# Kernel optimization log

Hardware: AMD Instinct MI355X
Metric: run time of the kernel (lower is better)

## Reference

```python
import jax, jax.numpy as jnp
import numpy as np

EMBED_DIM = 2048
NUM_HEADS = 16
HEAD_DIM = EMBED_DIM // NUM_HEADS
SEQ_LEN = 2048
ROPE_BASE = 10000.0


def rope_cache(seq_len, dim, base=ROPE_BASE):
    inv_freq = 1.0 / (base ** (jnp.arange(0, dim, 2, dtype=jnp.float32) / dim))
    t = jnp.arange(seq_len, dtype=jnp.float32)
    freqs = jnp.einsum('s,d->sd', t, inv_freq)  # [S, D/2]
    return jnp.cos(freqs), jnp.sin(freqs)


def apply_rope_interleaved(x, cos, sin):
    # x: [B, S, H, D]; interleaved pairs (even, odd)
    B, S, H, D = x.shape
    xp = x.reshape(B, S, H, D // 2, 2)
    x1, x2 = xp[..., 0], xp[..., 1]
    c = cos[None, :, None, :]
    s = sin[None, :, None, :]
    o1 = x1 * c - x2 * s
    o2 = x1 * s + x2 * c
    return jnp.stack([o1, o2], axis=-1).reshape(B, S, H, D)


def setup_inputs() -> dict:
    key = jax.random.key(0)
    ks = jax.random.split(key, 5)
    B = 2
    scale = 0.02
    x = jax.random.normal(ks[0], (B, SEQ_LEN, EMBED_DIM), dtype=jnp.float32)
    Wq = jax.random.normal(ks[1], (EMBED_DIM, EMBED_DIM), dtype=jnp.float32) * scale
    Wk = jax.random.normal(ks[2], (EMBED_DIM, EMBED_DIM), dtype=jnp.float32) * scale
    Wv = jax.random.normal(ks[3], (EMBED_DIM, EMBED_DIM), dtype=jnp.float32) * scale
    Wo = jax.random.normal(ks[4], (EMBED_DIM, EMBED_DIM), dtype=jnp.float32) * scale
    return {"x": x, "Wq": Wq, "Wk": Wk, "Wv": Wv, "Wo": Wo}


def reference(x, Wq, Wk, Wv, Wo):
    B, S, E = x.shape
    H, D = NUM_HEADS, HEAD_DIM
    # projections (nn.Linear: y = x @ W.T; here W stored as [out, in])
    q = (x @ Wq.T).reshape(B, S, H, D)
    k = (x @ Wk.T).reshape(B, S, H, D)
    v = (x @ Wv.T).reshape(B, S, H, D)
    cos, sin = rope_cache(S, D)
    q = apply_rope_interleaved(q, cos, sin)
    k = apply_rope_interleaved(k, cos, sin)
    # causal attention, flash-attn semantics: scale = head_dim**-0.5, fp32 softmax
    scale = 1.0 / jnp.sqrt(jnp.float32(D))
    scores = jnp.einsum('bqhd,bkhd->bhqk', q, k) * scale
    causal = jnp.tril(jnp.ones((S, S), dtype=bool))
    scores = jnp.where(causal[None, None], scores, jnp.float32(-jnp.inf))
    probs = jax.nn.softmax(scores.astype(jnp.float32), axis=-1)
    attn = jnp.einsum('bhqk,bkhd->bqhd', probs.astype(v.dtype), v)
    attn = attn.reshape(B, S, H * D)
    return attn @ Wo.T
```

## Files before the change

kernel.cpp:

```cpp
#include <hip/hip_runtime.h>
#include <cstdint>
#include <cmath>

typedef short s16x8 __attribute__((ext_vector_type(8)));
typedef float f32x4 __attribute__((ext_vector_type(4)));
typedef float f32x16 __attribute__((ext_vector_type(16)));
typedef int   i32x4 __attribute__((ext_vector_type(4)));
typedef unsigned short u16;

#define E_DIM 2048
#define SEQ   2048
#define NB    2
#define NH    16
#define HD    128
#define BS_TOT 4096

__device__ __forceinline__ u16 f2bf(float f) {
  unsigned u = __float_as_uint(f);
  u += 0x7fffu + ((u >> 16) & 1u);
  return (u16)(u >> 16);
}
__device__ __forceinline__ float bf2f(u16 h) {
  return __uint_as_float(((unsigned)h) << 16);
}
__device__ __forceinline__ float rmax16(float v) {
  v = fmaxf(v, __shfl_xor(v, 1));
  v = fmaxf(v, __shfl_xor(v, 2));
  v = fmaxf(v, __shfl_xor(v, 4));
  v = fmaxf(v, __shfl_xor(v, 8));
  return v;
}
__device__ __forceinline__ float rsum16(float v) {
  v += __shfl_xor(v, 1);
  v += __shfl_xor(v, 2);
  v += __shfl_xor(v, 4);
  v += __shfl_xor(v, 8);
  return v;
}

__device__ __forceinline__ void gll16(const u16* g, u16* l) {
  __builtin_amdgcn_global_load_lds(
      (const __attribute__((address_space(1))) void*)g,
      (__attribute__((address_space(3))) void*)l, 16, 0, 0);
}

__global__ __launch_bounds__(256) void cast_kernel(const float* __restrict__ in,
                                                   u16* __restrict__ out) {
  const size_t t = (size_t)blockIdx.x * 256 + threadIdx.x;
  const float* p = in + t * 8;
  f32x4 a = *(const f32x4*)p;
  f32x4 b = *(const f32x4*)(p + 4);
  union { u16 u[8]; i32x4 v; } r;
  r.u[0] = f2bf(a[0]); r.u[1] = f2bf(a[1]); r.u[2] = f2bf(a[2]); r.u[3] = f2bf(a[3]);
  r.u[4] = f2bf(b[0]); r.u[5] = f2bf(b[1]); r.u[6] = f2bf(b[2]); r.u[7] = f2bf(b[3]);
  *(i32x4*)(out + t * 8) = r.v;
}

__global__ __launch_bounds__(256) void cast2_kernel(const float* __restrict__ in0,
                                                    u16* __restrict__ out0,
                                                    const float* __restrict__ in1,
                                                    u16* __restrict__ out1,
                                                    int half) {
  const int bsel = blockIdx.x >= half;
  const float* in = bsel ? in1 : in0;
  u16* out = bsel ? out1 : out0;
  const size_t t = (size_t)(blockIdx.x - (bsel ? half : 0)) * 256 + threadIdx.x;
  const float* p = in + t * 8;
  f32x4 a = *(const f32x4*)p;
  f32x4 b = *(const f32x4*)(p + 4);
  union { u16 u[8]; i32x4 v; } r;
  r.u[0] = f2bf(a[0]); r.u[1] = f2bf(a[1]); r.u[2] = f2bf(a[2]); r.u[3] = f2bf(a[3]);
  r.u[4] = f2bf(b[0]); r.u[5] = f2bf(b[1]); r.u[6] = f2bf(b[2]); r.u[7] = f2bf(b[3]);
  *(i32x4*)(out + t * 8) = r.v;
}

template <typename OT, bool CVTA>
__global__ __launch_bounds__(256) void gemm_nt(const void* __restrict__ Av,
                                               const u16* __restrict__ B,
                                               OT* __restrict__ C,
                                               int M, int N, int K) {
  __shared__ __align__(16) u16 As[128 * 64];
  __shared__ __align__(16) u16 Bs[128 * 64];
  const int t  = threadIdx.x;
  const int w  = t >> 6, l = t & 63;
  const int l31 = l & 31, lh = l >> 5;
  const int wr = w >> 1, wc = w & 1;
  const int m0 = blockIdx.y * 128, n0 = blockIdx.x * 128;

  f32x16 acc[2][2];
#pragma unroll
  for (int mi = 0; mi < 2; ++mi)
#pragma unroll
    for (int ni = 0; ni < 2; ++ni)
#pragma unroll
      for (int e = 0; e < 16; ++e) acc[mi][ni][e] = 0.f;

  for (int k0 = 0; k0 < K; k0 += 64) {
    __syncthreads();
    if constexpr (CVTA) {
      const float* A = (const float*)Av;
#pragma unroll
      for (int i = 0; i < 4; ++i) {
        const int ci = i * 256 + t;
        const int r = ci >> 3, c = ci & 7, gq = c ^ (r & 7);
        const float* s = A + (size_t)(m0 + r) * K + k0 + gq * 8;
        f32x4 a = *(const f32x4*)s;
        f32x4 b = *(const f32x4*)(s + 4);
        union { u16 u[8]; i32x4 v; } rr;
        rr.u[0] = f2bf(a[0]); rr.u[1] = f2bf(a[1]); rr.u[2] = f2bf(a[2]); rr.u[3] = f2bf(a[3]);
        rr.u[4] = f2bf(b[0]); rr.u[5] = f2bf(b[1]); rr.u[6] = f2bf(b[2]); rr.u[7] = f2bf(b[3]);
        *(i32x4*)(As + ci * 8) = rr.v;
      }
    } else {
      const u16* A = (const u16*)Av;
#pragma unroll
      for (int i = 0; i < 4; ++i) {
        const int ci = i * 256 + t;
        const int r = ci >> 3, c = ci & 7, gq = c ^ (r & 7);
        gll16(A + (size_t)(m0 + r) * K + k0 + gq * 8, As + ci * 8);
      }
    }
#pragma unroll
    for (int i = 0; i < 4; ++i) {
      const int ci = i * 256 + t;
      const int r = ci >> 3, c = ci & 7, gq = c ^ (r & 7);
      gll16(B + (size_t)(n0 + r) * K + k0 + gq * 8, Bs + ci * 8);
    }
    __syncthreads();
#pragma unroll
    for (int ks = 0; ks < 4; ++ks) {
      const int chunk = ks * 2 + lh;
      s16x8 af[2], bf[2];
#pragma unroll
      for (int mi = 0; mi < 2; ++mi) {
        const int ra = wr * 64 + mi * 32 + l31;
        af[mi] = *(const s16x8*)(As + ra * 64 + ((chunk ^ (ra & 7)) << 3));
      }
#pragma unroll
      for (int ni = 0; ni < 2; ++ni) {
        const int rb = wc * 64 + ni * 32 + l31;
        bf[ni] = *(const s16x8*)(Bs + rb * 64 + ((chunk ^ (rb & 7)) << 3));
      }
#pragma unroll
      for (int mi = 0; mi < 2; ++mi)
#pragma unroll
        for (int ni = 0; ni < 2; ++ni)
          acc[mi][ni] = __builtin_amdgcn_mfma_f32_32x32x16_bf16(af[mi], bf[ni], acc[mi][ni], 0, 0, 0);
    }
  }

#pragma unroll
  for (int mi = 0; mi < 2; ++mi)
#pragma unroll
    for (int ni = 0; ni < 2; ++ni) {
      const int col = n0 + wc * 64 + ni * 32 + l31;
#pragma unroll
      for (int reg = 0; reg < 16; ++reg) {
        const int row = m0 + wr * 64 + mi * 32 + 4 * lh + (reg & 3) + 8 * (reg >> 2);
        const float v = acc[mi][ni][reg];
        if constexpr (sizeof(OT) == 2) {
          C[(size_t)row * N + col] = (OT)f2bf(v);
        } else {
          C[(size_t)row * N + col] = v;
        }
      }
    }
}

__global__ __launch_bounds__(256) void gemm_qk(const u16* __restrict__ A,
                                               const u16* __restrict__ B0,
                                               const u16* __restrict__ B1,
                                               u16* __restrict__ C0,
                                               u16* __restrict__ C1) {
  constexpr int K = 2048, N = 2048;
  __shared__ __align__(16) u16 As[128 * 64];
  __shared__ __align__(16) u16 Bs[128 * 64];
  const int bx = blockIdx.x;
  const u16* B = (bx >> 4) ? B1 : B0;
  u16* C = (bx >> 4) ? C1 : C0;
  const int n0 = (bx & 15) * 128, m0 = blockIdx.y * 128;
  const int t  = threadIdx.x;
  const int w  = t >> 6, l = t & 63;
  const int l31 = l & 31, lh = l >> 5;
  const int wr = w >> 1, wc = w & 1;

  f32x16 acc[2][2];
#pragma unroll
  for (int mi = 0; mi < 2; ++mi)
#pragma unroll
    for (int ni = 0; ni < 2; ++ni)
#pragma unroll
      for (int e = 0; e < 16; ++e) acc[mi][ni][e] = 0.f;

  for (int k0 = 0; k0 < K; k0 += 64) {
    __syncthreads();
#pragma unroll
    for (int i = 0; i < 4; ++i) {
      const int ci = i * 256 + t;
      const int r = ci >> 3, c = ci & 7, gq = c ^ (r & 7);
      gll16(A + (size_t)(m0 + r) * K + k0 + gq * 8, As + ci * 8);
    }
#pragma unroll
    for (int i = 0; i < 4; ++i) {
      const int ci = i * 256 + t;
      const int r = ci >> 3, c = ci & 7, gq = c ^ (r & 7);
      gll16(B + (size_t)(n0 + r) * K + k0 + gq * 8, Bs + ci * 8);
    }
    __syncthreads();
#pragma unroll
    for (int ks = 0; ks < 4; ++ks) {
      const int chunk = ks * 2 + lh;
      s16x8 af[2], bf[2];
#pragma unroll
      for (int mi = 0; mi < 2; ++mi) {
        const int ra = wr * 64 + mi * 32 + l31;
        af[mi] = *(const s16x8*)(As + ra * 64 + ((chunk ^ (ra & 7)) << 3));
      }
#pragma unroll
      for (int ni = 0; ni < 2; ++ni) {
        const int rb = wc * 64 + ni * 32 + l31;
        bf[ni] = *(const s16x8*)(Bs + rb * 64 + ((chunk ^ (rb & 7)) << 3));
      }
#pragma unroll
      for (int mi = 0; mi < 2; ++mi)
#pragma unroll
        for (int ni = 0; ni < 2; ++ni)
          acc[mi][ni] = __builtin_amdgcn_mfma_f32_32x32x16_bf16(af[mi], bf[ni], acc[mi][ni], 0, 0, 0);
    }
  }

#pragma unroll
  for (int mi = 0; mi < 2; ++mi)
#pragma unroll
    for (int ni = 0; ni < 2; ++ni) {
      const int col = n0 + wc * 64 + ni * 32 + l31;
#pragma unroll
      for (int reg = 0; reg < 16; ++reg) {
        const int row = m0 + wr * 64 + mi * 32 + 4 * lh + (reg & 3) + 8 * (reg >> 2);
        C[(size_t)row * N + col] = f2bf(acc[mi][ni][reg]);
      }
    }
}

__global__ __launch_bounds__(256) void rope_kernel(u16* __restrict__ q, u16* __restrict__ k) {
  const float QS = 0.08838834764831845f * 1.4426950408889634f;
  const size_t t = (size_t)blockIdx.x * 256 + threadIdx.x;
  const size_t e8 = t * 8;
  const int col = (int)(e8 & (E_DIM - 1));
  const int row = (int)(e8 >> 11);
  const int s   = row & (SEQ - 1);
  const int d   = col & (HD - 1);
  float cs[4], sn[4];
#pragma unroll
  for (int j = 0; j < 4; ++j) {
    const float inv = exp2f(-0.20762050593046014f * (float)((d >> 1) + j));
    const float ang = (float)s * inv;
    sincosf(ang, &sn[j], &cs[j]);
  }
  u16* qp = q + e8;
  u16* kp = k + e8;
  union { u16 u[8]; i32x4 v; } a, b;
  a.v = *(const i32x4*)qp;
  b.v = *(const i32x4*)kp;
#pragma unroll
  for (int j = 0; j < 4; ++j) {
    const float csq = cs[j] * QS, snq = sn[j] * QS;
    const float q1 = bf2f(a.u[2 * j]), q2 = bf2f(a.u[2 * j + 1]);
    const float k1 = bf2f(b.u[2 * j]), k2 = bf2f(b.u[2 * j + 1]);
    a.u[2 * j]     = f2bf(q1 * csq - q2 * snq);
    a.u[2 * j + 1] = f2bf(q1 * snq + q2 * csq);
    b.u[2 * j]     = f2bf(k1 * cs[j] - k2 * sn[j]);
    b.u[2 * j + 1] = f2bf(k1 * sn[j] + k2 * cs[j]);
  }
  *(i32x4*)qp = a.v;
  *(i32x4*)kp = b.v;
}

__global__ __launch_bounds__(512, 2) void flash_kernel(const u16* __restrict__ q,
                                                       const u16* __restrict__ kmat,
                                                       const u16* __restrict__ vt,
                                                       u16* __restrict__ attn) {
  __shared__ __align__(16) u16 KV[73728];
  const int bx = blockIdx.x;
  const int j  = bx >> 5;
  const int bh = (bx & 7) * 4 + ((bx >> 3) & 3);
  const int b  = bh >> 4, h = bh & 15;
  const int t = threadIdx.x, w = t >> 6, l = t & 63, lq = l >> 4, lm = l & 15;

  u16* Pw = KV + 65536 + w * 1024;
  const u16* kbase = kmat + (size_t)(b * SEQ) * E_DIM + h * HD;
  const u16* vbase = vt + (size_t)(h * HD) * BS_TOT + (size_t)b * SEQ;
  const f32x4 fzero = {0.f, 0.f, 0.f, 0.f};

  auto stage = [&](int it) {
    const int base = (it & 1) << 15;
    const int k0 = it * 128;
#pragma unroll
    for (int i = 0; i < 4; ++i) {
      const int ci = i * 512 + t;
      const int r = ci >> 4, gq = (ci & 15) ^ (r & 15);
      gll16(kbase + (size_t)(k0 + r) * E_DIM + gq * 8, KV + base + ci * 8);
    }
#pragma unroll
    for (int i = 0; i < 4; ++i) {
      const int ci = i * 512 + t;
      const int r = ci >> 4, gq = (ci & 15) ^ (r & 15);
      gll16(vbase + (size_t)r * BS_TOT + k0 + gq * 8, KV + base + 16384 + ci * 8);
    }
  };

  for (int pass = 0; pass < 2; ++pass) {
    const int qt = pass ? j : (15 - j);
    const int q0 = qt * 128;
    const int nT = qt + 1;

    stage(0);

    const u16* qp = q + (size_t)(b * SEQ + q0 + w * 16) * E_DIM + h * HD;
    s16x8 qf[4];
#pragma unroll
    for (int kx = 0; kx < 4; ++kx)
      qf[kx] = *(const s16x8*)(qp + (size_t)lm * E_DIM + kx * 32 + lq * 8);

    float m_i[4], l_i[4];
    f32x4 acc_o[8];
#pragma unroll
    for (int rr = 0; rr < 4; ++rr) { m_i[rr] = -1e30f; l_i[rr] = 0.f; }
#pragma unroll
    for (int nd = 0; nd < 8; ++nd) acc_o[nd] = fzero;

    for (int it = 0; it < nT; ++it) {
      const int base = (it & 1) << 15;
      const int k0 = it * 128;
      if (it + 1 < nT) {
        stage(it + 1);
        asm volatile("s_waitcnt vmcnt(8)" ::: "memory");
      } else {
        asm volatile("s_waitcnt vmcnt(0)" ::: "memory");
      }
      asm volatile("s_barrier" ::: "memory");

      f32x4 sc[8];
#pragma unroll
      for (int ni = 0; ni < 8; ++ni) sc[ni] = fzero;
      __builtin_amdgcn_s_setprio(1);
#pragma unroll
      for (int kx = 0; kx < 4; ++kx) {
        s16x8 kf[8];
#pragma unroll
        for (int ni = 0; ni < 8; ++ni) {
          const int rn = ni * 16 + lm;
          kf[ni] = *(const s16x8*)(KV + base + rn * 128 + (((kx * 4 + lq) ^ lm) << 3));
        }
#pragma unroll
        for (int ni = 0; ni < 8; ++ni)
          sc[ni] = __builtin_amdgcn_mfma_f32_16x16x32_bf16(qf[kx], kf[ni], sc[ni], 0, 0, 0);
      }
      __builtin_amdgcn_s_setprio(0);

      const bool diag = (it == nT - 1);
#pragma unroll
      for (int rr = 0; rr < 4; ++rr) {
        const int qrow = q0 + w * 16 + lq * 4 + rr;
        float mt = -1e30f;
#pragma unroll
        for (int ni = 0; ni < 8; ++ni) {
          float s = sc[ni][rr];
          if (diag && (k0 + ni * 16 + lm) > qrow) s = -1e30f;
          sc[ni][rr] = s;
          mt = fmaxf(mt, s);
        }
        mt = rmax16(mt);
        const float mn = fmaxf(m_i[rr], mt);
        const float al = exp2f(m_i[rr] - mn);
        float rs = 0.f;
#pragma unroll
        for (int ni = 0; ni < 8; ++ni) {
          const float p = exp2f(sc[ni][rr] - mn);
          sc[ni][rr] = p;
          rs += p;
        }
        rs = rsum16(rs);
        l_i[rr] = l_i[rr] * al + rs;
        m_i[rr] = mn;
#pragma unroll
        for (int nd = 0; nd < 8; ++nd) acc_o[nd][rr] *= al;
      }

      __builtin_amdgcn_s_setprio(1);
#pragma unroll
      for (int half = 0; half < 2; ++half) {
#pragma unroll
        for (int rr = 0; rr < 4; ++rr) {
          const int r = lq * 4 + rr;
#pragma unroll
          for (int ni = 0; ni < 4; ++ni) {
            const int c = ni * 16 + lm;
            Pw[r * 64 + (((c >> 3) ^ (r & 7)) << 3) + (c & 7)] =
                f2bf(sc[half * 4 + ni][rr]);
          }
        }
#pragma unroll
        for (int kx = 0; kx < 2; ++kx) {
          const s16x8 pf = *(const s16x8*)(Pw + lm * 64 + (((kx * 4 + lq) ^ (lm & 7)) << 3));
#pragma unroll
          for (int nd = 0; nd < 8; ++nd) {
            const int rn = nd * 16 + lm;
            const s16x8 vf = *(const s16x8*)(KV + base + 16384 + rn * 128 +
                                             (((half * 8 + kx * 4 + lq) ^ lm) << 3));
            acc_o[nd] = __builtin_amdgcn_mfma_f32_16x16x32_bf16(pf, vf, acc_o[nd], 0, 0, 0);
          }
        }
      }
      __builtin_amdgcn_s_setprio(0);

      asm volatile("s_barrier" ::: "memory");
    }

    u16* op = attn + (size_t)(b * SEQ + q0 + w * 16) * E_DIM + h * HD;
#pragma unroll
    for (int rr = 0; rr < 4; ++rr) {
      const float inv = 1.0f / l_i[rr];
      const int row = lq * 4 + rr;
#pragma unroll
      for (int nd = 0; nd < 8; ++nd) {
        const int colc = nd * 16 + lm;
        op[(size_t)row * E_DIM + colc] = f2bf(acc_o[nd][rr] * inv);
      }
    }
  }
}

extern "C" void kernel_launch(void* const* d_in, const int* in_sizes, int n_in,
                              void* d_out, int out_size, void* d_ws, size_t ws_size,
                              hipStream_t stream) {
  const float* x  = (const float*)d_in[0];
  const float* Wq = (const float*)d_in[1];
  const float* Wk = (const float*)d_in[2];
  const float* Wv = (const float*)d_in[3];
  const float* Wo = (const float*)d_in[4];
  float* out = (float*)d_out;
  char* ws = (char*)d_ws;

  u16* xb    = (u16*)(ws);
  u16* vslot = (u16*)(ws + (size_t)16 * 1048576);
  u16* wq_bf = vslot;
  u16* wk_bf = vslot + (size_t)4 * 1048576;
  u16* vtb   = vslot;
  u16* wo_bf = vslot;
  u16* qb    = (u16*)d_out;
  u16* kb    = (u16*)d_out + (size_t)8 * 1048576;
  u16* attnb = xb;

  (void)in_sizes; (void)n_in; (void)out_size; (void)ws_size;

  cast_kernel<<<4096, 256, 0, stream>>>(x, xb);
  cast2_kernel<<<4096, 256, 0, stream>>>(Wq, wq_bf, Wk, wk_bf, 2048);
  gemm_qk<<<dim3(32, 32), 256, 0, stream>>>(xb, wq_bf, wk_bf, qb, kb);
  gemm_nt<u16, true><<<dim3(32, 16), 256, 0, stream>>>(Wv, xb, vtb, 2048, 4096, 2048);
  rope_kernel<<<4096, 256, 0, stream>>>(qb, kb);
  flash_kernel<<<256, 512, 0, stream>>>(qb, kb, vtb, attnb);
  cast_kernel<<<2048, 256, 0, stream>>>(Wo, wo_bf);
  gemm_nt<float, false><<<dim3(16, 32), 256, 0, stream>>>(attnb, wo_bf, out, 4096, 2048, 2048);
}
```

Baseline: 420.5 us.

## Double-buffer LDS in projection GEMMs and merge cast launches

The projection GEMMs move to two LDS buffers and prefetch the next K tile while the current one is multiplied. They use explicit vmcnt waits and s_barrier in place of two __syncthreads per iteration. In the fp32-A path the global loads are kept in registers and converted to bf16 after the MFMAs. The x and Wq/Wk casts are merged into one three-way launch. This doubles LDS use, which may lower occupancy, and relies on hand-tuned waitcnt values being correct.

New measurement: 404.7 us. -3.7%, faster.

```diff
diff --git a/kernel.cpp b/kernel.cpp
--- a/kernel.cpp
+++ b/kernel.cpp
@@ -56,15 +56,19 @@
   *(i32x4*)(out + t * 8) = r.v;
 }
 
-__global__ __launch_bounds__(256) void cast2_kernel(const float* __restrict__ in0,
+__global__ __launch_bounds__(256) void cast3_kernel(const float* __restrict__ in0,
                                                     u16* __restrict__ out0,
                                                     const float* __restrict__ in1,
                                                     u16* __restrict__ out1,
-                                                    int half) {
-  const int bsel = blockIdx.x >= half;
-  const float* in = bsel ? in1 : in0;
-  u16* out = bsel ? out1 : out0;
-  const size_t t = (size_t)(blockIdx.x - (bsel ? half : 0)) * 256 + threadIdx.x;
+                                                    const float* __restrict__ in2,
+                                                    u16* __restrict__ out2,
+                                                    int n0, int n1) {
+  const int bx = blockIdx.x;
+  const float* in; u16* out; int bb;
+  if (bx < n0)           { in = in0; out = out0; bb = bx; }
+  else if (bx < n0 + n1) { in = in1; out = out1; bb = bx - n0; }
+  else                   { in = in2; out = out2; bb = bx - n0 - n1; }
+  const size_t t = (size_t)bb * 256 + threadIdx.x;
   const float* p = in + t * 8;
   f32x4 a = *(const f32x4*)p;
   f32x4 b = *(const f32x4*)(p + 4);
@@ -79,74 +83,116 @@
                                                const u16* __restrict__ B,
                                                OT* __restrict__ C,
                                                int M, int N, int K) {
-  __shared__ __align__(16) u16 As[128 * 64];
-  __shared__ __align__(16) u16 Bs[128 * 64];
+  __shared__ __align__(16) u16 As[2][128 * 64];
+  __shared__ __align__(16) u16 Bs[2][128 * 64];
   const int t  = threadIdx.x;
   const int w  = t >> 6, l = t & 63;
   const int l31 = l & 31, lh = l >> 5;
   const int wr = w >> 1, wc = w & 1;
   const int m0 = blockIdx.y * 128, n0 = blockIdx.x * 128;
-
-  f32x16 acc[2][2];
-#pragma unroll
-  for (int mi = 0; mi < 2; ++mi)
-#pragma unroll
-    for (int ni = 0; ni < 2; ++ni)
-#pragma unroll
-      for (int e = 0; e < 16; ++e) acc[mi][ni][e] = 0.f;
-
-  for (int k0 = 0; k0 < K; k0 += 64) {
-    __syncthreads();
-    if constexpr (CVTA) {
-      const float* A = (const float*)Av;
-#pragma unroll
-      for (int i = 0; i < 4; ++i) {
-        const int ci = i * 256 + t;
-        const int r = ci >> 3, c = ci & 7, gq = c ^ (r & 7);
-        const float* s = A + (size_t)(m0 + r) * K + k0 + gq * 8;
-        f32x4 a = *(const f32x4*)s;
-        f32x4 b = *(const f32x4*)(s + 4);
-        union { u16 u[8]; i32x4 v; } rr;
-        rr.u[0] = f2bf(a[0]); rr.u[1] = f2bf(a[1]); rr.u[2] = f2bf(a[2]); rr.u[3] = f2bf(a[3]);
-        rr.u[4] = f2bf(b[0]); rr.u[5] = f2bf(b[1]); rr.u[6] = f2bf(b[2]); rr.u[7] = f2bf(b[3]);
-        *(i32x4*)(As + ci * 8) = rr.v;
-      }
-    } else {
-      const u16* A = (const u16*)Av;
-#pragma unroll
-      for (int i = 0; i < 4; ++i) {
-        const int ci = i * 256 + t;
-        const int r = ci >> 3, c = ci & 7, gq = c ^ (r & 7);
-        gll16(A + (size_t)(m0 + r) * K + k0 + gq * 8, As + ci * 8);
-      }
-    }
+  const int nIt = K >> 6;
+
+  f32x4 pa[4], pb[4];
+
+  auto stageB = [&](int it) {
+    const int k0 = it << 6, sb = it & 1;
 #pragma unroll
     for (int i = 0; i < 4; ++i) {
       const int ci = i * 256 + t;
       const int r = ci >> 3, c = ci & 7, gq = c ^ (r & 7);
-      gll16(B + (size_t)(n0 + r) * K + k0 + gq * 8, Bs + ci * 8);
-    }
-    __syncthreads();
+      gll16(B + (size_t)(n0 + r) * K + k0 + gq * 8, Bs[sb] + ci * 8);
+    }
+  };
+  auto stageA = [&](int it) {
+    const u16* A = (const u16*)Av;
+    const int k0 = it << 6, sb = it & 1;
+#pragma unroll
+    for (int i = 0; i < 4; ++i) {
+      const int ci = i * 256 + t;
+      const int r = ci >> 3, c = ci & 7, gq = c ^ (r & 7);
+      gll16(A + (size_t)(m0 + r) * K + k0 + gq * 8, As[sb] + ci * 8);
+    }
+  };
+  auto loadA = [&](int it) {
+    const float* A = (const float*)Av;
+    const int k0 = it << 6;
+#pragma unroll
+    for (int i = 0; i < 4; ++i) {
+      const int ci = i * 256 + t;
+      const int r = ci >> 3, c = ci & 7, gq = c ^ (r & 7);
+      const float* s = A + (size_t)(m0 + r) * K + k0 + gq * 8;
+      pa[i] = *(const f32x4*)s;
+      pb[i] = *(const f32x4*)(s + 4);
+    }
+  };
+  auto writeA = [&](int it) {
+    const int sb = it & 1;
+#pragma unroll
+    for (int i = 0; i < 4; ++i) {
+      const int ci = i * 256 + t;
+      union { u16 u[8]; i32x4 v; } rr;
+      rr.u[0] = f2bf(pa[i][0]); rr.u[1] = f2bf(pa[i][1]);
+      rr.u[2] = f2bf(pa[i][2]); rr.u[3] = f2bf(pa[i][3]);
+      rr.u[4] = f2bf(pb[i][0]); rr.u[5] = f2bf(pb[i][1]);
+      rr.u[6] = f2bf(pb[i][2]); rr.u[7] = f2bf(pb[i][3]);
+      *(i32x4*)(As[sb] + ci * 8) = rr.v;
+    }
+  };
+
+  f32x16 acc[2][2];
+#pragma unroll
+  for (int mi = 0; mi < 2; ++mi)
+#pragma unroll
+    for (int ni = 0; ni < 2; ++ni)
+#pragma unroll
+      for (int e = 0; e < 16; ++e) acc[mi][ni][e] = 0.f;
+
+  if constexpr (CVTA) { loadA(0); stageB(0); writeA(0); }
+  else                { stageA(0); stageB(0); }
+
+  for (int it = 0; it < nIt; ++it) {
+    const int cb = it & 1;
+    if (it + 1 < nIt) {
+      if constexpr (CVTA) {
+        loadA(it + 1); stageB(it + 1);
+        asm volatile("s_waitcnt vmcnt(12) lgkmcnt(0)" ::: "memory");
+      } else {
+        stageA(it + 1); stageB(it + 1);
+        asm volatile("s_waitcnt vmcnt(8)" ::: "memory");
+      }
+    } else {
+      asm volatile("s_waitcnt vmcnt(0) lgkmcnt(0)" ::: "memory");
+    }
+    asm volatile("s_barrier" ::: "memory");
+
+    const u16* Ab = As[cb];
+    const u16* Bb = Bs[cb];
 #pragma unroll
     for (int ks = 0; ks < 4; ++ks) {
       const int chunk = ks * 2 + lh;
-      s16x8 af[2], bf[2];
+      s16x8 af[2], bfr[2];
 #pragma unroll
       for (int mi = 0; mi < 2; ++mi) {
         const int ra = wr * 64 + mi * 32 + l31;
-        af[mi] = *(const s16x8*)(As + ra * 64 + ((chunk ^ (ra & 7)) << 3));
+        af[mi] = *(const s16x8*)(Ab + ra * 64 + ((chunk ^ (ra & 7)) << 3));
       }
 #pragma unroll
       for (int ni = 0; ni < 2; ++ni) {
         const int rb = wc * 64 + ni * 32 + l31;
-        bf[ni] = *(const s16x8*)(Bs + rb * 64 + ((chunk ^ (rb & 7)) << 3));
+        bfr[ni] = *(const s16x8*)(Bb + rb * 64 + ((chunk ^ (rb & 7)) << 3));
       }
 #pragma unroll
       for (int mi = 0; mi < 2; ++mi)
 #pragma unroll
         for (int ni = 0; ni < 2; ++ni)
-          acc[mi][ni] = __builtin_amdgcn_mfma_f32_32x32x16_bf16(af[mi], bf[ni], acc[mi][ni], 0, 0, 0);
-    }
+          acc[mi][ni] = __builtin_amdgcn_mfma_f32_32x32x16_bf16(af[mi], bfr[ni], acc[mi][ni], 0, 0, 0);
+    }
+
+    if constexpr (CVTA) {
+      if (it + 1 < nIt) writeA(it + 1);
+      asm volatile("s_waitcnt lgkmcnt(0)" ::: "memory");
+    }
+    asm volatile("s_barrier" ::: "memory");
   }
 
 #pragma unroll
@@ -173,8 +219,9 @@
                                                u16* __restrict__ C0,
                                                u16* __restrict__ C1) {
   constexpr int K = 2048, N = 2048;
-  __shared__ __align__(16) u16 As[128 * 64];
-  __shared__ __align__(16) u16 Bs[128 * 64];
+  constexpr int nIt = K >> 6;
+  __shared__ __align__(16) u16 As[2][128 * 64];
+  __shared__ __align__(16) u16 Bs[2][128 * 64];
   const int bx = blockIdx.x;
   const u16* B = (bx >> 4) ? B1 : B0;
   u16* C = (bx >> 4) ? C1 : C0;
@@ -184,49 +231,66 @@
   const int l31 = l & 31, lh = l >> 5;
   const int wr = w >> 1, wc = w & 1;
 
-  f32x16 acc[2][2];
-#pragma unroll
-  for (int mi = 0; mi < 2; ++mi)
-#pragma unroll
-    for (int ni = 0; ni < 2; ++ni)
-#pragma unroll
-      for (int e = 0; e < 16; ++e) acc[mi][ni][e] = 0.f;
-
-  for (int k0 = 0; k0 < K; k0 += 64) {
-    __syncthreads();
+  auto stage = [&](int it) {
+    const int k0 = it << 6, sb = it & 1;
 #pragma unroll
     for (int i = 0; i < 4; ++i) {
       const int ci = i * 256 + t;
       const int r = ci >> 3, c = ci & 7, gq = c ^ (r & 7);
-      gll16(A + (size_t)(m0 + r) * K + k0 + gq * 8, As + ci * 8);
+      gll16(A + (size_t)(m0 + r) * K + k0 + gq * 8, As[sb] + ci * 8);
     }
 #pragma unroll
     for (int i = 0; i < 4; ++i) {
       const int ci = i * 256 + t;
       const int r = ci >> 3, c = ci & 7, gq = c ^ (r & 7);
-      gll16(B + (size_t)(n0 + r) * K + k0 + gq * 8, Bs + ci * 8);
-    }
-    __syncthreads();
+      gll16(B + (size_t)(n0 + r) * K + k0 + gq * 8, Bs[sb] + ci * 8);
+    }
+  };
+
+  f32x16 acc[2][2];
+#pragma unroll
+  for (int mi = 0; mi < 2; ++mi)
+#pragma unroll
+    for (int ni = 0; ni < 2; ++ni)
+#pragma unroll
+      for (int e = 0; e < 16; ++e) acc[mi][ni][e] = 0.f;
+
+  stage(0);
+
+  for (int it = 0; it < nIt; ++it) {
+    const int cb = it & 1;
+    if (it + 1 < nIt) {
+      stage(it + 1);
+      asm volatile("s_waitcnt vmcnt(8)" ::: "memory");
+    } else {
+      asm volatile("s_waitcnt vmcnt(0)" ::: "memory");
+    }
+    asm volatile("s_barrier" ::: "memory");
+
+    const u16* Ab = As[cb];
+    const u16* Bb = Bs[cb];
 #pragma unroll
     for (int ks = 0; ks < 4; ++ks) {
       const int chunk = ks * 2 + lh;
-      s16x8 af[2], bf[2];
+      s16x8 af[2], bfr[2];
 #pragma unroll
       for (int mi = 0; mi < 2; ++mi) {
         const int ra = wr * 64 + mi * 32 + l31;
-        af[mi] = *(const s16x8*)(As + ra * 64 + ((chunk ^ (ra & 7)) << 3));
+        af[mi] = *(const s16x8*)(Ab + ra * 64 + ((chunk ^ (ra & 7)) << 3));
       }
 #pragma unroll
       for (int ni = 0; ni < 2; ++ni) {
         const int rb = wc * 64 + ni * 32 + l31;
-        bf[ni] = *(const s16x8*)(Bs + rb * 64 + ((chunk ^ (rb & 7)) << 3));
+        bfr[ni] = *(const s16x8*)(Bb + rb * 64 + ((chunk ^ (rb & 7)) << 3));
       }
 #pragma unroll
       for (int mi = 0; mi < 2; ++mi)
 #pragma unroll
         for (int ni = 0; ni < 2; ++ni)
-          acc[mi][ni] = __builtin_amdgcn_mfma_f32_32x32x16_bf16(af[mi], bf[ni], acc[mi][ni], 0, 0, 0);
-    }
+          acc[mi][ni] = __builtin_amdgcn_mfma_f32_32x32x16_bf16(af[mi], bfr[ni], acc[mi][ni], 0, 0, 0);
+    }
+
+    asm volatile("s_barrier" ::: "memory");
   }
 
 #pragma unroll
@@ -454,8 +518,7 @@
 
   (void)in_sizes; (void)n_in; (void)out_size; (void)ws_size;
 
-  cast_kernel<<<4096, 256, 0, stream>>>(x, xb);
-  cast2_kernel<<<4096, 256, 0, stream>>>(Wq, wq_bf, Wk, wk_bf, 2048);
+  cast3_kernel<<<8192, 256, 0, stream>>>(x, xb, Wq, wq_bf, Wk, wk_bf, 4096, 2048);
   gemm_qk<<<dim3(32, 32), 256, 0, stream>>>(xb, wq_bf, wk_bf, qb, kb);
   gemm_nt<u16, true><<<dim3(32, 16), 256, 0, stream>>>(Wv, xb, vtb, 2048, 4096, 2048);
   rope_kernel<<<4096, 256, 0, stream>>>(qb, kb);
```
